# Kernel tuning notes

Measured on AMD Instinct MI355X. Metric: run time of the kernel, lower is better.

## Reference

```python
import jax, jax.numpy as jnp
import numpy as np

T, H, I, E, TOPK = 2048, 2048, 1408, 8, 2


def setup_inputs() -> dict:
    key = jax.random.key(0)
    k1, k2, k3, k4 = jax.random.split(key, 4)
    x = jax.random.normal(k1, (T, H), dtype=jnp.float32)
    router_logits = jax.random.normal(k2, (T, E), dtype=jnp.float32)
    # scale weights down so activations stay well-conditioned
    w13_weight = jax.random.normal(k3, (E, 2 * I, H), dtype=jnp.float32) * (1.0 / np.sqrt(H))
    w2_weight = jax.random.normal(k4, (E, H, I), dtype=jnp.float32) * (1.0 / np.sqrt(I))
    return {"x": x, "router_logits": router_logits, "w13_weight": w13_weight,
            "w2_weight": w2_weight, "top_k": TOPK}


def reference(x, router_logits, w13_weight, w2_weight, top_k):
    # --- select_experts: softmax scoring, top-k, renormalize ---
    probs = jax.nn.softmax(router_logits.astype(jnp.float32), axis=-1)   # [T, E]
    topk_w, topk_ids = jax.lax.top_k(probs, top_k)                        # [T, k]
    topk_w = topk_w / jnp.sum(topk_w, axis=-1, keepdims=True)             # renormalize
    topk_w = topk_w.astype(x.dtype)

    n_tok = x.shape[0]
    n_exp = w13_weight.shape[0]
    inter = w2_weight.shape[2]

    # dense combine weights [T, E]: zero for unselected experts
    comb = jnp.zeros((n_tok, n_exp), dtype=x.dtype)
    comb = comb.at[jnp.arange(n_tok)[:, None], topk_ids].add(topk_w)

    # --- fused_experts: gated SiLU MLP per expert, weighted combine ---
    gate_up = jnp.einsum('th,eih->tei', x, w13_weight)                    # [T, E, 2I]
    gate, up = gate_up[..., :inter], gate_up[..., inter:]
    act = jax.nn.silu(gate) * up                                          # [T, E, I]
    out = jnp.einsum('tei,ehi,te->th', act, w2_weight, comb)              # [T, H]
    return out
```

## Files before the change

kernel.cpp:

```cpp
#include <hip/hip_runtime.h>
#include <hip/hip_bf16.h>
#include <stdint.h>

#define T_TOK 2048
#define H_DIM 2048
#define I_DIM 1408
#define NEXP  8
#define NPOS  4096
#define NPAD  5120
#define MAXT  40

typedef short short8 __attribute__((ext_vector_type(8)));
typedef float f32x4  __attribute__((ext_vector_type(4)));

__device__ __forceinline__ short f2bf(float f) {
  union { float f; uint32_t u; } v; v.f = f;
  uint32_t r = (v.u + 0x7FFFu + ((v.u >> 16) & 1u)) >> 16;
  return (short)r;
}
__device__ __forceinline__ float bf2f(short s) {
  union { uint32_t u; float f; } v; v.u = ((uint32_t)(uint16_t)s) << 16;
  return v.f;
}

__device__ __forceinline__ short8 cvt8(f32x4 a, f32x4 b) {
  __hip_bfloat162 h0 = __float22bfloat162_rn(float2{a[0], a[1]});
  __hip_bfloat162 h1 = __float22bfloat162_rn(float2{a[2], a[3]});
  __hip_bfloat162 h2 = __float22bfloat162_rn(float2{b[0], b[1]});
  __hip_bfloat162 h3 = __float22bfloat162_rn(float2{b[2], b[3]});
  short2 s0, s1, s2, s3;
  __builtin_memcpy(&s0, &h0, 4); __builtin_memcpy(&s1, &h1, 4);
  __builtin_memcpy(&s2, &h2, 4); __builtin_memcpy(&s3, &h3, 4);
  short8 r;
  r[0] = s0.x; r[1] = s0.y; r[2] = s1.x; r[3] = s1.y;
  r[4] = s2.x; r[5] = s2.y; r[6] = s3.x; r[7] = s3.y;
  return r;
}

__device__ __forceinline__ void load_lds16(const void* g, void* l) {
  __builtin_amdgcn_global_load_lds((const __attribute__((address_space(1))) uint32_t*)g,
                                   (__attribute__((address_space(3))) uint32_t*)l,
                                   16, 0, 0);
}

__global__ void k_routing(const float* __restrict__ logits,
                          int* __restrict__ pos_token,
                          float* __restrict__ pos_w,
                          int* __restrict__ eoff,
                          int* __restrict__ inv) {
  __shared__ int   s_ids[T_TOK];
  __shared__ float s_w0[T_TOK];
  __shared__ float s_w1[T_TOK];
  __shared__ int s_cnt[NEXP], s_cur[NEXP], s_off[NEXP + 1];
  const int tid = threadIdx.x;
  if (tid < NEXP) { s_cnt[tid] = 0; s_cur[tid] = 0; }
  for (int p = tid; p < NPAD; p += blockDim.x) { pos_token[p] = 0; pos_w[p] = 0.f; }
  __syncthreads();

  for (int t = tid; t < T_TOK; t += blockDim.x) {
    float l[NEXP];
#pragma unroll
    for (int e = 0; e < NEXP; ++e) l[e] = logits[t * NEXP + e];
    int b0 = 0; float v0 = l[0];
#pragma unroll
    for (int e = 1; e < NEXP; ++e) if (l[e] > v0) { v0 = l[e]; b0 = e; }
    int b1 = -1; float v1 = -1e30f;
#pragma unroll
    for (int e = 0; e < NEXP; ++e) if (e != b0 && l[e] > v1) { v1 = l[e]; b1 = e; }
    float t1 = __expf(v1 - v0);
    float w0 = 1.f / (1.f + t1);
    float w1 = 1.f - w0;
    s_ids[t] = b0 | (b1 << 8);
    s_w0[t] = w0; s_w1[t] = w1;
    atomicAdd(&s_cnt[b0], 1);
    atomicAdd(&s_cnt[b1], 1);
  }
  __syncthreads();
  if (tid == 0) {
    int acc = 0;
    for (int e = 0; e < NEXP; ++e) {
      s_off[e] = acc;
      acc += (s_cnt[e] + 127) & ~127;
    }
    s_off[NEXP] = acc;
    for (int e = 0; e <= NEXP; ++e) eoff[e] = s_off[e];
  }
  __syncthreads();
  for (int t = tid; t < T_TOK; t += blockDim.x) {
    int ids = s_ids[t];
    int e0 = ids & 255, e1 = ids >> 8;
    int p0 = s_off[e0] + atomicAdd(&s_cur[e0], 1);
    pos_token[p0] = t; pos_w[p0] = s_w0[t];
    int p1 = s_off[e1] + atomicAdd(&s_cur[e1], 1);
    pos_token[p1] = t; pos_w[p1] = s_w1[t];
    inv[2 * t] = p0; inv[2 * t + 1] = p1;
  }
}

__global__ void k_gather(const float* __restrict__ x,
                         const int* __restrict__ pos_token,
                         short* __restrict__ xg) {
  const int p = blockIdx.x;
  const int tid = threadIdx.x;
  const int tok = pos_token[p];
  const f32x4* src = (const f32x4*)(x + (size_t)tok * H_DIM);
  f32x4 a = src[tid * 2];
  f32x4 b = src[tid * 2 + 1];
  ((short8*)(xg + (size_t)p * H_DIM))[tid] = cvt8(a, b);
}

__device__ __forceinline__ int tile_expert(const int* eoff, int row0) {
  int e = 0;
#pragma unroll
  for (int i = 1; i < NEXP; ++i) if (row0 >= eoff[i]) e = i;
  return e;
}

__global__ __launch_bounds__(256, 5) void k_gateup(
    const short* __restrict__ xg, const float* __restrict__ w13,
    const int* __restrict__ eoff, short* __restrict__ act) {
  __shared__ __align__(16) short a_s[2][128 * 32];
  __shared__ __align__(16) short bg_s[2][64 * 32];
  __shared__ __align__(16) short bu_s[2][64 * 32];

  int bxr = blockIdx.x;
  const int bx = (bxr & 7) * 110 + (bxr >> 3);
  const int tile = bx / 22;
  const int nt = bx - tile * 22;
  const int row0 = tile * 128;
  if (row0 >= eoff[NEXP]) return;
  const int e = tile_expert(eoff, row0);

  const int tid = threadIdx.x;
  const int wid = tid >> 6;
  const int lane = tid & 63;
  const int wm = wid >> 1, wn = wid & 1;

  f32x4 accg[4][2] = {};
  f32x4 accu[4][2] = {};

  const short* aG  = xg + (size_t)row0 * H_DIM;
  const float* bgG = w13 + (size_t)e * (2 * I_DIM) * H_DIM + (size_t)(nt * 64) * H_DIM;
  const float* buG = bgG + (size_t)I_DIM * H_DIM;

  const int row  = tid >> 2;
  const int scol = ((tid & 3) ^ ((tid >> 3) & 3)) * 8;

  auto stageA = [&](int t, int bi) {
    const int ks = t * 32;
    load_lds16(aG + (size_t)row * H_DIM + ks + scol,        (char*)a_s[bi] + wid * 1024);
    load_lds16(aG + (size_t)(64 + row) * H_DIM + ks + scol, (char*)a_s[bi] + 4096 + wid * 1024);
  };

  f32x4 g0, g1, u0, u1;
  auto ldB = [&](int t) {
    const int ks = t * 32;
    const float* sg = bgG + (size_t)row * H_DIM + ks + scol;
    const float* su = buG + (size_t)row * H_DIM + ks + scol;
    g0 = *(const f32x4*)sg; g1 = *(const f32x4*)(sg + 4);
    u0 = *(const f32x4*)su; u1 = *(const f32x4*)(su + 4);
  };
  auto wrB = [&](int bi) {
    *(short8*)((char*)bg_s[bi] + tid * 16) = cvt8(g0, g1);
    *(short8*)((char*)bu_s[bi] + tid * 16) = cvt8(u0, u1);
  };

  auto compute = [&](int bi) {
    const int asl = ((lane >> 4) ^ ((lane >> 1) & 3)) * 16;
    short8 af[4];
#pragma unroll
    for (int fm = 0; fm < 4; ++fm) {
      int m = wm * 64 + fm * 16 + (lane & 15);
      af[fm] = *(const short8*)((const char*)a_s[bi] + m * 64 + asl);
    }
#pragma unroll
    for (int fn = 0; fn < 2; ++fn) {
      int n = wn * 32 + fn * 16 + (lane & 15);
      short8 bg = *(const short8*)((const char*)bg_s[bi] + n * 64 + asl);
      short8 bu = *(const short8*)((const char*)bu_s[bi] + n * 64 + asl);
#pragma unroll
      for (int fm = 0; fm < 4; ++fm)
        accg[fm][fn] = __builtin_amdgcn_mfma_f32_16x16x32_bf16(af[fm], bg, accg[fm][fn], 0, 0, 0);
#pragma unroll
      for (int fm = 0; fm < 4; ++fm)
        accu[fm][fn] = __builtin_amdgcn_mfma_f32_16x16x32_bf16(af[fm], bu, accu[fm][fn], 0, 0, 0);
    }
  };

  const int NK = H_DIM / 32;
  stageA(0, 0); ldB(0); wrB(0);
  __syncthreads();
  for (int t = 0; t < NK; ++t) {
    int bi = t & 1;
    if (t + 1 < NK) { stageA(t + 1, bi ^ 1); ldB(t + 1); }
    compute(bi);
    if (t + 1 < NK) wrB(bi ^ 1);
    __syncthreads();
  }

#pragma unroll
  for (int fm = 0; fm < 4; ++fm) {
#pragma unroll
    for (int rr = 0; rr < 4; ++rr) {
      int m = wm * 64 + fm * 16 + (lane >> 4) * 4 + rr;
      size_t grow = (size_t)(row0 + m);
#pragma unroll
      for (int fn = 0; fn < 2; ++fn) {
        int col = nt * 64 + wn * 32 + fn * 16 + (lane & 15);
        float g = accg[fm][fn][rr];
        float u = accu[fm][fn][rr];
        float a = g / (1.f + __expf(-g)) * u;
        act[grow * I_DIM + col] = f2bf(a);
      }
    }
  }
}

__global__ __launch_bounds__(256, 3) void k_down(
    const short* __restrict__ act, const float* __restrict__ w2,
    const int* __restrict__ eoff, short* __restrict__ y) {
  __shared__ __align__(16) short a_s[2][128 * 32];
  __shared__ __align__(16) short b_s[2][128 * 32];

  int bxr = blockIdx.x;
  const int bx = (bxr & 7) * 80 + (bxr >> 3);
  const int tile = bx >> 4;
  const int nt = bx & 15;
  const int row0 = tile * 128;
  if (row0 >= eoff[NEXP]) return;
  const int e = tile_expert(eoff, row0);

  const int tid = threadIdx.x;
  const int wid = tid >> 6;
  const int lane = tid & 63;
  const int wm = wid >> 1, wn = wid & 1;

  f32x4 acc[4][4] = {};

  const short* aG = act + (size_t)row0 * I_DIM;
  const float* bG = w2 + (size_t)e * H_DIM * I_DIM + (size_t)(nt * 128) * I_DIM;

  const int row  = tid >> 2;
  const int scol = ((tid & 3) ^ ((tid >> 3) & 3)) * 8;

  auto stageA = [&](int t, int bi) {
    const int ks = t * 32;
    load_lds16(aG + (size_t)row * I_DIM + ks + scol,        (char*)a_s[bi] + wid * 1024);
    load_lds16(aG + (size_t)(64 + row) * I_DIM + ks + scol, (char*)a_s[bi] + 4096 + wid * 1024);
  };
  auto ldB = [&](int t, f32x4& b00, f32x4& b01, f32x4& b10, f32x4& b11) {
    const int ks = t * 32;
    const float* s0 = bG + (size_t)row * I_DIM + ks + scol;
    const float* s1 = bG + (size_t)(64 + row) * I_DIM + ks + scol;
    b00 = *(const f32x4*)s0; b01 = *(const f32x4*)(s0 + 4);
    b10 = *(const f32x4*)s1; b11 = *(const f32x4*)(s1 + 4);
  };
  auto wrB = [&](int bi, f32x4& b00, f32x4& b01, f32x4& b10, f32x4& b11) {
    *(short8*)((char*)b_s[bi] + tid * 16)        = cvt8(b00, b01);
    *(short8*)((char*)b_s[bi] + 4096 + tid * 16) = cvt8(b10, b11);
  };

  auto compute = [&](int bi) {
    const int asl = ((lane >> 4) ^ ((lane >> 1) & 3)) * 16;
    short8 af[4];
#pragma unroll
    for (int fm = 0; fm < 4; ++fm) {
      int m = wm * 64 + fm * 16 + (lane & 15);
      af[fm] = *(const short8*)((const char*)a_s[bi] + m * 64 + asl);
    }
#pragma unroll
    for (int fn = 0; fn < 4; ++fn) {
      int n = wn * 64 + fn * 16 + (lane & 15);
      short8 bb = *(const short8*)((const char*)b_s[bi] + n * 64 + asl);
#pragma unroll
      for (int fm = 0; fm < 4; ++fm)
        acc[fm][fn] = __builtin_amdgcn_mfma_f32_16x16x32_bf16(af[fm], bb, acc[fm][fn], 0, 0, 0);
    }
  };

  const int NK = I_DIM / 32;
  f32x4 e0, e1, e2, e3, o0, o1, o2, o3;

  stageA(0, 0);
  ldB(0, e0, e1, e2, e3);
  wrB(0, e0, e1, e2, e3);
  ldB(1, e0, e1, e2, e3);
  ldB(2, o0, o1, o2, o3);
  __syncthreads();

#define DN_STEP(T, B0, B1, B2, B3)                                            \
  {                                                                           \
    const int t_ = (T);                                                       \
    const int bi_ = t_ & 1;                                                   \
    const int tn_ = (t_ + 1 < NK) ? t_ + 1 : NK - 1;                          \
    const int tf_ = (t_ + 3 < NK) ? t_ + 3 : NK - 1;                          \
    stageA(tn_, bi_ ^ 1);                                                     \
    __builtin_amdgcn_sched_barrier(0);                                        \
    wrB(bi_ ^ 1, B0, B1, B2, B3);                                             \
    ldB(tf_, B0, B1, B2, B3);                                                 \
    compute(bi_);                                                             \
    asm volatile("s_waitcnt vmcnt(4) lgkmcnt(0)" ::: "memory");               \
    __builtin_amdgcn_s_barrier();                                             \
  }
  for (int tp = 0; tp < NK; tp += 2) {
    DN_STEP(tp,     e0, e1, e2, e3);
    DN_STEP(tp + 1, o0, o1, o2, o3);
  }
#undef DN_STEP
  asm volatile("s_waitcnt vmcnt(0)" ::: "memory");

#pragma unroll
  for (int fm = 0; fm < 4; ++fm) {
#pragma unroll
    for (int rr = 0; rr < 4; ++rr) {
      int m = wm * 64 + fm * 16 + (lane >> 4) * 4 + rr;
      size_t grow = (size_t)(row0 + m);
#pragma unroll
      for (int fn = 0; fn < 4; ++fn) {
        int col = nt * 128 + wn * 64 + fn * 16 + (lane & 15);
        y[grow * H_DIM + col] = f2bf(acc[fm][fn][rr]);
      }
    }
  }
}

__global__ void k_combine(const short* __restrict__ y,
                          const int* __restrict__ inv,
                          const float* __restrict__ pos_w,
                          float* __restrict__ out) {
  const int t = blockIdx.x;
  const int tid = threadIdx.x;
  const int p0 = inv[2 * t], p1 = inv[2 * t + 1];
  const float w0 = pos_w[p0], w1 = pos_w[p1];
  short8 a = ((const short8*)(y + (size_t)p0 * H_DIM))[tid];
  short8 b = ((const short8*)(y + (size_t)p1 * H_DIM))[tid];
  f32x4 r0, r1;
#pragma unroll
  for (int j = 0; j < 4; ++j) {
    r0[j] = w0 * bf2f(a[j]) + w1 * bf2f(b[j]);
    r1[j] = w0 * bf2f(a[j + 4]) + w1 * bf2f(b[j + 4]);
  }
  f32x4* o = (f32x4*)(out + (size_t)t * H_DIM);
  o[tid * 2]     = r0;
  o[tid * 2 + 1] = r1;
}

extern "C" void kernel_launch(void* const* d_in, const int* in_sizes, int n_in,
                              void* d_out, int out_size, void* d_ws, size_t ws_size,
                              hipStream_t stream) {
  const float* x      = (const float*)d_in[0];
  const float* logits = (const float*)d_in[1];
  const float* w13    = (const float*)d_in[2];
  const float* w2     = (const float*)d_in[3];
  (void)in_sizes; (void)n_in; (void)out_size; (void)ws_size;
  float* out = (float*)d_out;
  char* ws = (char*)d_ws;

  size_t o = 0;
  auto alloc = [&](size_t bytes) { size_t r = o; o += (bytes + 255) & ~(size_t)255; return r; };
  short* xg        = (short*)(ws + alloc((size_t)NPAD * H_DIM * 2));
  short* act       = (short*)(ws + alloc((size_t)NPAD * I_DIM * 2));
  short* y         = (short*)(ws + alloc((size_t)NPAD * H_DIM * 2));
  int*   pos_token = (int*)  (ws + alloc((size_t)NPAD * 4));
  float* pos_w     = (float*)(ws + alloc((size_t)NPAD * 4));
  int*   inv       = (int*)  (ws + alloc((size_t)T_TOK * 2 * 4));
  int*   eoff      = (int*)  (ws + alloc((NEXP + 1) * 4));

  k_routing<<<1, 1024, 0, stream>>>(logits, pos_token, pos_w, eoff, inv);
  k_gather<<<NPAD, 256, 0, stream>>>(x, pos_token, xg);
  k_gateup<<<MAXT * 22, 256, 0, stream>>>(xg, w13, eoff, act);
  k_down<<<MAXT * 16, 256, 0, stream>>>(act, w2, eoff, y);
  k_combine<<<T_TOK, 256, 0, stream>>>(y, inv, pos_w, out);
}
```

Baseline: 238.6 us.

## Enlarge gate-up tiles to 256 rows with 512 threads and deeper B prefetch

The gate-up GEMM now processes 256-row tiles with 512 threads, so each fp32 weight tile loaded and converted to bf16 is reused across twice as many tokens. Expert padding is raised to 256 rows and the workspace and grid sizes grow to match. The K loop is unrolled by two with register-held B prefetch three steps ahead and manual waitcnt/barrier control. Stores of padded rows are skipped, but padding can add wasted MMA work, and the down kernel now runs over more padded tiles.

Result: slower. 249.7 us (+4.6%).

```diff
diff --git a/kernel.cpp b/kernel.cpp
--- a/kernel.cpp
+++ b/kernel.cpp
@@ -5,11 +5,13 @@
 #define T_TOK 2048
 #define H_DIM 2048
 #define I_DIM 1408
+#define GU_W  2816
 #define NEXP  8
 #define NPOS  4096
-#define NPAD  5120
-#define MAXT  40
-
+#define NPAD  6144
+#define MAXT  48
+
+typedef short short4v __attribute__((ext_vector_type(4)));
 typedef short short8 __attribute__((ext_vector_type(8)));
 typedef float f32x4  __attribute__((ext_vector_type(4)));
 
@@ -34,6 +36,14 @@
   short8 r;
   r[0] = s0.x; r[1] = s0.y; r[2] = s1.x; r[3] = s1.y;
   r[4] = s2.x; r[5] = s2.y; r[6] = s3.x; r[7] = s3.y;
+  return r;
+}
+__device__ __forceinline__ short4v cvt4(f32x4 a) {
+  __hip_bfloat162 h0 = __float22bfloat162_rn(float2{a[0], a[1]});
+  __hip_bfloat162 h1 = __float22bfloat162_rn(float2{a[2], a[3]});
+  short2 s0, s1;
+  __builtin_memcpy(&s0, &h0, 4); __builtin_memcpy(&s1, &h1, 4);
+  short4v r; r[0] = s0.x; r[1] = s0.y; r[2] = s1.x; r[3] = s1.y;
   return r;
 }
 
@@ -80,7 +90,7 @@
     int acc = 0;
     for (int e = 0; e < NEXP; ++e) {
       s_off[e] = acc;
-      acc += (s_cnt[e] + 127) & ~127;
+      acc += (s_cnt[e] + 255) & ~255;
     }
     s_off[NEXP] = acc;
     for (int e = 0; e <= NEXP; ++e) eoff[e] = s_off[e];
@@ -116,53 +126,57 @@
   return e;
 }
 
-__global__ __launch_bounds__(256, 5) void k_gateup(
+__global__ __launch_bounds__(512, 2) void k_gateup(
     const short* __restrict__ xg, const float* __restrict__ w13,
     const int* __restrict__ eoff, short* __restrict__ act) {
-  __shared__ __align__(16) short a_s[2][128 * 32];
+  __shared__ __align__(16) short a_s[2][256 * 32];
   __shared__ __align__(16) short bg_s[2][64 * 32];
   __shared__ __align__(16) short bu_s[2][64 * 32];
 
-  int bxr = blockIdx.x;
-  const int bx = (bxr & 7) * 110 + (bxr >> 3);
+  const int bxr = blockIdx.x;
+  const int bx = (bxr & 7) * 66 + (bxr >> 3);
   const int tile = bx / 22;
   const int nt = bx - tile * 22;
-  const int row0 = tile * 128;
+  const int row0 = tile * 256;
   if (row0 >= eoff[NEXP]) return;
   const int e = tile_expert(eoff, row0);
+  const int end = eoff[e + 1];
 
   const int tid = threadIdx.x;
   const int wid = tid >> 6;
   const int lane = tid & 63;
   const int wm = wid >> 1, wn = wid & 1;
 
+  const float* bgG = w13 + (size_t)e * GU_W * H_DIM + (size_t)(nt * 64) * H_DIM;
+  const float* buG = bgG + (size_t)I_DIM * H_DIM;
+
+  const int brow = tid >> 3;
+  const int bg16 = (tid >> 1) & 3;
+  const int bh   = tid & 1;
+  const int bsc  = ((bg16 ^ ((brow >> 1) & 3)) * 8 + bh * 4);
+
   f32x4 accg[4][2] = {};
   f32x4 accu[4][2] = {};
 
-  const short* aG  = xg + (size_t)row0 * H_DIM;
-  const float* bgG = w13 + (size_t)e * (2 * I_DIM) * H_DIM + (size_t)(nt * 64) * H_DIM;
-  const float* buG = bgG + (size_t)I_DIM * H_DIM;
-
-  const int row  = tid >> 2;
-  const int scol = ((tid & 3) ^ ((tid >> 3) & 3)) * 8;
-
   auto stageA = [&](int t, int bi) {
     const int ks = t * 32;
-    load_lds16(aG + (size_t)row * H_DIM + ks + scol,        (char*)a_s[bi] + wid * 1024);
-    load_lds16(aG + (size_t)(64 + row) * H_DIM + ks + scol, (char*)a_s[bi] + 4096 + wid * 1024);
-  };
-
-  f32x4 g0, g1, u0, u1;
-  auto ldB = [&](int t) {
+#pragma unroll
+    for (int i = 0; i < 2; ++i) {
+      const int s = i * 512 + tid;
+      const int row = s >> 2;
+      const int sc  = ((s & 3) ^ ((s >> 3) & 3)) * 8;
+      load_lds16(xg + (size_t)(row0 + row) * H_DIM + ks + sc,
+                 (char*)a_s[bi] + i * 8192 + wid * 1024);
+    }
+  };
+  auto ldB = [&](int t, f32x4& g, f32x4& u) {
     const int ks = t * 32;
-    const float* sg = bgG + (size_t)row * H_DIM + ks + scol;
-    const float* su = buG + (size_t)row * H_DIM + ks + scol;
-    g0 = *(const f32x4*)sg; g1 = *(const f32x4*)(sg + 4);
-    u0 = *(const f32x4*)su; u1 = *(const f32x4*)(su + 4);
-  };
-  auto wrB = [&](int bi) {
-    *(short8*)((char*)bg_s[bi] + tid * 16) = cvt8(g0, g1);
-    *(short8*)((char*)bu_s[bi] + tid * 16) = cvt8(u0, u1);
+    g = *(const f32x4*)(bgG + (size_t)brow * H_DIM + ks + bsc);
+    u = *(const f32x4*)(buG + (size_t)brow * H_DIM + ks + bsc);
+  };
+  auto wrB = [&](int bi, f32x4& g, f32x4& u) {
+    *(short4v*)((char*)bg_s[bi] + tid * 8) = cvt4(g);
+    *(short4v*)((char*)bu_s[bi] + tid * 8) = cvt4(u);
   };
 
   auto compute = [&](int bi) {
@@ -188,29 +202,51 @@
   };
 
   const int NK = H_DIM / 32;
-  stageA(0, 0); ldB(0); wrB(0);
+  f32x4 gE, uE, gO, uO;
+
+  stageA(0, 0);
+  ldB(0, gE, uE);
+  wrB(0, gE, uE);
+  ldB(1, gE, uE);
+  ldB(2, gO, uO);
   __syncthreads();
-  for (int t = 0; t < NK; ++t) {
-    int bi = t & 1;
-    if (t + 1 < NK) { stageA(t + 1, bi ^ 1); ldB(t + 1); }
-    compute(bi);
-    if (t + 1 < NK) wrB(bi ^ 1);
-    __syncthreads();
-  }
+
+#define GU_STEP(T, G, U)                                                      \
+  {                                                                           \
+    const int t_ = (T);                                                       \
+    const int bi_ = t_ & 1;                                                   \
+    const int tn_ = (t_ + 1 < NK) ? t_ + 1 : NK - 1;                          \
+    const int tf_ = (t_ + 3 < NK) ? t_ + 3 : NK - 1;                          \
+    stageA(tn_, bi_ ^ 1);                                                     \
+    __builtin_amdgcn_sched_barrier(0);                                        \
+    wrB(bi_ ^ 1, G, U);                                                       \
+    ldB(tf_, G, U);                                                           \
+    compute(bi_);                                                             \
+    asm volatile("s_waitcnt vmcnt(2) lgkmcnt(0)" ::: "memory");               \
+    __builtin_amdgcn_s_barrier();                                             \
+  }
+  for (int tp = 0; tp < NK; tp += 2) {
+    GU_STEP(tp,     gE, uE);
+    GU_STEP(tp + 1, gO, uO);
+  }
+#undef GU_STEP
+  asm volatile("s_waitcnt vmcnt(0)" ::: "memory");
 
 #pragma unroll
   for (int fm = 0; fm < 4; ++fm) {
 #pragma unroll
     for (int rr = 0; rr < 4; ++rr) {
       int m = wm * 64 + fm * 16 + (lane >> 4) * 4 + rr;
-      size_t grow = (size_t)(row0 + m);
-#pragma unroll
-      for (int fn = 0; fn < 2; ++fn) {
-        int col = nt * 64 + wn * 32 + fn * 16 + (lane & 15);
-        float g = accg[fm][fn][rr];
-        float u = accu[fm][fn][rr];
-        float a = g / (1.f + __expf(-g)) * u;
-        act[grow * I_DIM + col] = f2bf(a);
+      int grow = row0 + m;
+      if (grow < end) {
+#pragma unroll
+        for (int fn = 0; fn < 2; ++fn) {
+          int col = nt * 64 + wn * 32 + fn * 16 + (lane & 15);
+          float g = accg[fm][fn][rr];
+          float u = accu[fm][fn][rr];
+          float a = g / (1.f + __expf(-g)) * u;
+          act[(size_t)grow * I_DIM + col] = f2bf(a);
+        }
       }
     }
   }
@@ -223,7 +259,7 @@
   __shared__ __align__(16) short b_s[2][128 * 32];
 
   int bxr = blockIdx.x;
-  const int bx = (bxr & 7) * 80 + (bxr >> 3);
+  const int bx = (bxr & 7) * 96 + (bxr >> 3);
   const int tile = bx >> 4;
   const int nt = bx & 15;
   const int row0 = tile * 128;
@@ -368,7 +404,7 @@
 
   k_routing<<<1, 1024, 0, stream>>>(logits, pos_token, pos_w, eoff, inv);
   k_gather<<<NPAD, 256, 0, stream>>>(x, pos_token, xg);
-  k_gateup<<<MAXT * 22, 256, 0, stream>>>(xg, w13, eoff, act);
+  k_gateup<<<528, 512, 0, stream>>>(xg, w13, eoff, act);
   k_down<<<MAXT * 16, 256, 0, stream>>>(act, w2, eoff, y);
   k_combine<<<T_TOK, 256, 0, stream>>>(y, inv, pos_w, out);
 }
```
